# Kernel optimization log

Hardware: AMD Instinct MI355X
Metric: run time of the kernel (lower is better)

## Reference

```python
import jax, jax.numpy as jnp
import numpy as np

B, C, H, W = 4, 128, 64, 64
CQ = C // 2  # channels // reduction_ratio


def setup_inputs() -> dict:
    key = jax.random.key(0)
    ks = jax.random.split(key, 7)
    # kaiming-normal-ish init for 1x1 conv weights (fan_in = C)
    std = float(np.sqrt(2.0 / C))
    return {
        "x": jax.random.normal(ks[0], (B, C, H, W), dtype=jnp.float32),
        "Wq": jax.random.normal(ks[1], (CQ, C), dtype=jnp.float32) * std,
        "bq": jnp.zeros((CQ,), dtype=jnp.float32),
        "Wk": jax.random.normal(ks[2], (CQ, C), dtype=jnp.float32) * std,
        "bk": jnp.zeros((CQ,), dtype=jnp.float32),
        "Wv": jax.random.normal(ks[3], (C, C), dtype=jnp.float32) * std,
        "bv": jnp.zeros((C,), dtype=jnp.float32),
    }


def reference(x, Wq, bq, Wk, bk, Wv, bv):
    b, c, h, w = x.shape
    n = h * w
    xf = x.reshape(b, c, n)  # [B, C, N]
    # 1x1 convs == channel matmuls
    q = jnp.einsum("oc,bcn->bon", Wq, xf) + bq[None, :, None]  # [B, Cq, N]
    k = jnp.einsum("oc,bcn->bon", Wk, xf) + bk[None, :, None]  # [B, Cq, N]
    v = jnp.einsum("oc,bcn->bon", Wv, xf) + bv[None, :, None]  # [B, C, N]
    # scores[b, i, j] = sum_c q[b, c, i] * k[b, c, j]
    scores = jnp.einsum("bci,bcj->bij", q, k)  # [B, N, N]
    probs = jax.nn.softmax(scores, axis=-1)
    # out[b, c, i] = sum_j v[b, c, j] * probs[b, i, j]
    out = jnp.einsum("bcj,bij->bci", v, probs)
    return out.reshape(b, c, h, w)
```

## Files before the change

kernel.cpp:

```cpp
#include <hip/hip_runtime.h>

#define Bn  4
#define Cn  128
#define CQn 64
#define Nn  4096

typedef _Float16 h8_t __attribute__((ext_vector_type(8)));
typedef __fp16   p2_t __attribute__((ext_vector_type(2)));
typedef float    f32x4 __attribute__((ext_vector_type(4)));
typedef unsigned int u32;


#define QKV_BYTES   8388608ull
#define PART_PER_S  4194304ull
#define ML_PER_S    131072ull
#define LOG2E       1.44269504f

__global__ __launch_bounds__(256) void qkv_proj(
    const float* __restrict__ x,
    const float* __restrict__ Wq, const float* __restrict__ bq,
    const float* __restrict__ Wk, const float* __restrict__ bk,
    const float* __restrict__ Wv, const float* __restrict__ bv,
    _Float16* __restrict__ Qh, _Float16* __restrict__ Kh, _Float16* __restrict__ Vg)
{
    __shared__ _Float16 XsT[64][136];

    const int nt   = blockIdx.x;
    const int ot   = blockIdx.y;
    const int b    = blockIdx.z;
    const int tid  = threadIdx.x;
    const int w    = tid >> 6;
    const int lane = tid & 63;
    const int g    = lane >> 4;
    const int ln   = lane & 15;
    const int nbase = nt * 64;

    const float* xb = x + (size_t)b * Cn * Nn + nbase;
    #pragma unroll
    for (int u = 0; u < 8; ++u) {
        int f  = tid + u * 256;
        int c  = f >> 4;
        int n4 = (f & 15) * 4;
        float4 v = *(const float4*)&xb[(size_t)c * Nn + n4];
        XsT[n4 + 0][c] = (_Float16)v.x;
        XsT[n4 + 1][c] = (_Float16)v.y;
        XsT[n4 + 2][c] = (_Float16)v.z;
        XsT[n4 + 3][c] = (_Float16)v.w;
    }
    __syncthreads();

    const float* Wsrc; const float* bsrc;
    if      (ot == 0) { Wsrc = Wq;            bsrc = bq;      }
    else if (ot == 1) { Wsrc = Wk;            bsrc = bk;      }
    else if (ot == 2) { Wsrc = Wv;            bsrc = bv;      }
    else              { Wsrc = Wv + 64 * Cn;  bsrc = bv + 64; }

    union H8 { h8_t h; _Float16 e[8]; };

    const int os = w;
    f32x4 acc[4];
    #pragma unroll
    for (int ns = 0; ns < 4; ++ns) acc[ns] = (f32x4){0.f, 0.f, 0.f, 0.f};

    #pragma unroll
    for (int kc = 0; kc < 4; ++kc) {
        const float* wp = Wsrc + (size_t)(os * 16 + ln) * Cn + kc * 32 + 8 * g;
        float4 wa = *(const float4*)wp;
        float4 wb = *(const float4*)(wp + 4);
        H8 t;
        t.e[0] = (_Float16)wa.x; t.e[1] = (_Float16)wa.y;
        t.e[2] = (_Float16)wa.z; t.e[3] = (_Float16)wa.w;
        t.e[4] = (_Float16)wb.x; t.e[5] = (_Float16)wb.y;
        t.e[6] = (_Float16)wb.z; t.e[7] = (_Float16)wb.w;
        const h8_t wf = t.h;
        #pragma unroll
        for (int ns = 0; ns < 4; ++ns) {
            const h8_t xv = *(const h8_t*)&XsT[ns * 16 + ln][kc * 32 + 8 * g];
            acc[ns] = __builtin_amdgcn_mfma_f32_16x16x32_f16(wf, xv, acc[ns], 0, 0, 0);
        }
    }

    if (ot <= 1) {
        union H4 { _Float16 e[4]; short4 s; };
        _Float16* dst = (ot == 0 ? Qh : Kh) + ((size_t)b * Nn + nbase) * CQn;
        const float sc = (ot == 0) ? LOG2E : 1.f;
        float4 bb = *(const float4*)&bsrc[os * 16 + 4 * g];
        #pragma unroll
        for (int ns = 0; ns < 4; ++ns) {
            H4 h;
            h.e[0] = (_Float16)((acc[ns][0] + bb.x) * sc);
            h.e[1] = (_Float16)((acc[ns][1] + bb.y) * sc);
            h.e[2] = (_Float16)((acc[ns][2] + bb.z) * sc);
            h.e[3] = (_Float16)((acc[ns][3] + bb.w) * sc);
            *(short4*)&dst[(size_t)(ns * 16 + ln) * CQn + os * 16 + 4 * g] = h.s;
        }
    } else {
        _Float16* dst = Vg + (size_t)(b * 64 + nt) * 8192;
        const int cbase = (ot - 2) * 64 + os * 16 + 4 * g;
        #pragma unroll
        for (int ns = 0; ns < 4; ++ns) {
            const int pos = 32 * (ns >> 1) + 8 * ((4 * ns + (ln >> 2)) & 3)
                          + 4 * (ns & 1) + (ln & 3);
            #pragma unroll
            for (int r = 0; r < 4; ++r) {
                dst[(size_t)(cbase + r) * 64 + pos] =
                    (_Float16)(acc[ns][r] + bsrc[os * 16 + 4 * g + r]);
            }
        }
    }
}

__device__ __forceinline__ void gload16(const void* g, void* l) {
    __builtin_amdgcn_global_load_lds(
        (const __attribute__((address_space(1))) u32*)g,
        (__attribute__((address_space(3))) u32*)l, 16, 0, 0);
}

#define KOFF0 0
#define KOFF1 8192
#define VOFF  16384

__global__ __launch_bounds__(256) void attn_split(
    const _Float16* __restrict__ Qh, const _Float16* __restrict__ Kh,
    const _Float16* __restrict__ Vg, float* __restrict__ out,
    _Float16* __restrict__ pPart, float* __restrict__ pMl, int S)
{
    __shared__ __align__(16) char smem[32768];

    const int tid  = threadIdx.x;
    const int w    = tid >> 6;
    const int lane = tid & 63;
    const int g    = lane >> 4;
    const int ln   = lane & 15;
    const int it   = blockIdx.x;
    const int b    = blockIdx.y;
    const int s    = blockIdx.z;
    const int wib  = it * 64 + w * 16;
    const int njt  = 64 / S;

    const _Float16* qrow = Qh + ((size_t)(b * Nn + wib + ln)) * CQn + 8 * g;
    const h8_t q0 = *(const h8_t*)(qrow);
    const h8_t q1 = *(const h8_t*)(qrow + 32);

    const _Float16* Kb  = Kh + (size_t)b * Nn * CQn;
    const _Float16* Vgb = Vg + (size_t)b * 64 * 8192;

    int ks[2];
    #pragma unroll
    for (int u = 0; u < 2; ++u) {
        int G   = u * 256 + tid;
        int row = G >> 3;
        ks[u] = row * CQn + (((G & 7) ^ (row & 7)) * 8);
    }
    int vs[4];
    #pragma unroll
    for (int u = 0; u < 4; ++u) {
        int G   = u * 256 + tid;
        int row = G >> 3;
        vs[u] = row * 64 + (((G & 7) ^ (row & 7)) * 8);
    }

    const int r7  = ln & 7;
    const int kb0 = ln * 128 + (((    g) ^ r7) << 4);
    const int kb1 = ln * 128 + (((4 + g) ^ r7) << 4);

    auto stageK = [&](int koff, int jt) {
        const _Float16* src = Kb + (size_t)jt * 64 * CQn;
        #pragma unroll
        for (int u = 0; u < 2; ++u)
            gload16(src + ks[u], smem + koff + u * 4096 + w * 1024);
    };
    auto stageV = [&](int jt) {
        const _Float16* src = Vgb + (size_t)jt * 8192;
        #pragma unroll
        for (int u = 0; u < 4; ++u)
            gload16(src + vs[u], smem + VOFF + u * 4096 + w * 1024);
    };

    f32x4 oacc[8];
    #pragma unroll
    for (int i = 0; i < 8; ++i) oacc[i] = (f32x4){0.f, 0.f, 0.f, 0.f};
    float m_run = -3.0e38f, l_run = 0.f;

    const int jt0 = s * njt;
    stageK(KOFF0, jt0);
    stageV(jt0);
    __syncthreads();

    for (int t = 0; t < njt; ++t) {
        if (t + 1 < njt) stageK((t & 1) ? KOFF0 : KOFF1, jt0 + t + 1);

        const char* KU = smem + ((t & 1) ? KOFF1 : KOFF0);
        f32x4 st[4];
        __builtin_amdgcn_s_setprio(1);
        #pragma unroll
        for (int js = 0; js < 4; ++js) {
            h8_t k0 = *(const h8_t*)(KU + kb0 + js * 2048);
            h8_t k1 = *(const h8_t*)(KU + kb1 + js * 2048);
            st[js] = (f32x4){0.f, 0.f, 0.f, 0.f};
            st[js] = __builtin_amdgcn_mfma_f32_16x16x32_f16(k0, q0, st[js], 0, 0, 0);
            st[js] = __builtin_amdgcn_mfma_f32_16x16x32_f16(k1, q1, st[js], 0, 0, 0);
        }
        __builtin_amdgcn_s_setprio(0);

        float tmax = st[0][0];
        #pragma unroll
        for (int js = 0; js < 4; ++js)
            #pragma unroll
            for (int r = 0; r < 4; ++r) tmax = fmaxf(tmax, st[js][r]);
        tmax = fmaxf(tmax, __shfl_xor(tmax, 16));
        tmax = fmaxf(tmax, __shfl_xor(tmax, 32));
        if (__any(tmax > m_run + 11.54f)) {
            const float mnew  = fmaxf(m_run, tmax);
            const float alpha = __builtin_amdgcn_exp2f(m_run - mnew);
            const float a0 = __shfl(alpha, 4 * g + 0);
            const float a1 = __shfl(alpha, 4 * g + 1);
            const float a2 = __shfl(alpha, 4 * g + 2);
            const float a3 = __shfl(alpha, 4 * g + 3);
            #pragma unroll
            for (int cs = 0; cs < 8; ++cs) {
                oacc[cs][0] *= a0; oacc[cs][1] *= a1;
                oacc[cs][2] *= a2; oacc[cs][3] *= a3;
            }
            l_run *= alpha;
            m_run = mnew;
        }
        float ts = 0.f;
        #pragma unroll
        for (int js = 0; js < 4; ++js)
            #pragma unroll
            for (int r = 0; r < 4; ++r) {
                float p = __builtin_amdgcn_exp2f(st[js][r] - m_run);
                st[js][r] = p;
                ts += p;
            }
        ts += __shfl_xor(ts, 16);
        ts += __shfl_xor(ts, 32);
        l_run += ts;

        union H8P { h8_t h; p2_t p2[4]; };
        H8P p0u, p1u;
        p0u.p2[0] = __builtin_amdgcn_cvt_pkrtz(st[0][0], st[0][1]);
        p0u.p2[1] = __builtin_amdgcn_cvt_pkrtz(st[0][2], st[0][3]);
        p0u.p2[2] = __builtin_amdgcn_cvt_pkrtz(st[1][0], st[1][1]);
        p0u.p2[3] = __builtin_amdgcn_cvt_pkrtz(st[1][2], st[1][3]);
        p1u.p2[0] = __builtin_amdgcn_cvt_pkrtz(st[2][0], st[2][1]);
        p1u.p2[1] = __builtin_amdgcn_cvt_pkrtz(st[2][2], st[2][3]);
        p1u.p2[2] = __builtin_amdgcn_cvt_pkrtz(st[3][0], st[3][1]);
        p1u.p2[3] = __builtin_amdgcn_cvt_pkrtz(st[3][2], st[3][3]);
        const h8_t pa0 = p0u.h;
        const h8_t pa1 = p1u.h;

        __syncthreads();

        __builtin_amdgcn_s_setprio(1);
        #pragma unroll
        for (int cs = 0; cs < 8; ++cs) {
            h8_t v01 = *(const h8_t*)(smem + VOFF + kb0 + cs * 2048);
            h8_t v23 = *(const h8_t*)(smem + VOFF + kb1 + cs * 2048);
            oacc[cs] = __builtin_amdgcn_mfma_f32_16x16x32_f16(pa0, v01, oacc[cs], 0, 0, 0);
            oacc[cs] = __builtin_amdgcn_mfma_f32_16x16x32_f16(pa1, v23, oacc[cs], 0, 0, 0);
        }
        __builtin_amdgcn_s_setprio(0);

        __syncthreads();

        if (t + 1 < njt) stageV(jt0 + t + 1);
    }

    const float lr = 1.f / l_run;
    const float l0 = __shfl(lr, 4 * g + 0);
    const float l1 = __shfl(lr, 4 * g + 1);
    const float l2 = __shfl(lr, 4 * g + 2);
    const float l3 = __shfl(lr, 4 * g + 3);

    if (S == 1) {
        float* ob = out + (size_t)b * Cn * Nn;
        #pragma unroll
        for (int cs = 0; cs < 8; ++cs) {
            float4 o;
            o.x = oacc[cs][0] * l0;
            o.y = oacc[cs][1] * l1;
            o.z = oacc[cs][2] * l2;
            o.w = oacc[cs][3] * l3;
            *(float4*)&ob[(size_t)(cs * 16 + ln) * Nn + wib + 4 * g] = o;
        }
    } else {
        union H4 { _Float16 e[4]; short4 sv; };
        _Float16* pp = pPart + (((size_t)b * 64 + it) * S + s) * 8192;
        const int qloc = w * 16 + 4 * g;
        #pragma unroll
        for (int cs = 0; cs < 8; ++cs) {
            H4 h;
            h.e[0] = (_Float16)(oacc[cs][0] * l0);
            h.e[1] = (_Float16)(oacc[cs][1] * l1);
            h.e[2] = (_Float16)(oacc[cs][2] * l2);
            h.e[3] = (_Float16)(oacc[cs][3] * l3);
            *(short4*)&pp[(size_t)(cs * 16 + ln) * 64 + qloc] = h.sv;
        }
        if (g == 0) {
            float* ml = pMl + ((((size_t)b * 64 + it) * S + s) * 64 + w * 16 + ln) * 2;
            ml[0] = m_run;
            ml[1] = l_run;
        }
    }
}

__global__ __launch_bounds__(256) void attn_combine(
    const _Float16* __restrict__ pPart, const float* __restrict__ pMl,
    float* __restrict__ out, int S)
{
    const int it  = blockIdx.x;
    const int b   = blockIdx.y;
    const int ch  = blockIdx.z;
    const int tid = threadIdx.x;

    __shared__ float wgt[4][64];
    __shared__ float linv[64];

    if (tid < 64) {
        const float* mlb = pMl + (((size_t)b * 64 + it) * S * 64 + tid) * 2;
        float ms[4], ls[4], m = -3.0e38f;
        for (int s = 0; s < S; ++s) {
            ms[s] = mlb[s * 128 + 0];
            ls[s] = mlb[s * 128 + 1];
            m = fmaxf(m, ms[s]);
        }
        float l = 0.f;
        for (int s = 0; s < S; ++s) {
            float wv = ls[s] * __builtin_amdgcn_exp2f(ms[s] - m);
            wgt[s][tid] = wv;
            l += wv;
        }
        linv[tid] = 1.f / l;
    }
    __syncthreads();

    const int c  = ch * 64 + (tid >> 2);
    const int q0 = (tid & 3) * 16;
    const _Float16* base = pPart + ((size_t)b * 64 + it) * S * 8192 + (size_t)c * 64 + q0;

    float acc[16];
    #pragma unroll
    for (int k = 0; k < 16; ++k) acc[k] = 0.f;
    for (int s = 0; s < S; ++s) {
        const _Float16* ps = base + (size_t)s * 8192;
        #pragma unroll
        for (int k = 0; k < 16; k += 8) {
            h8_t v = *(const h8_t*)(ps + k);
            #pragma unroll
            for (int j = 0; j < 8; ++j)
                acc[k + j] += wgt[s][q0 + k + j] * (float)v[j];
        }
    }
    float* ob = out + ((size_t)b * Cn + c) * Nn + it * 64 + q0;
    #pragma unroll
    for (int k = 0; k < 16; k += 4) {
        float4 o;
        o.x = acc[k + 0] * linv[q0 + k + 0];
        o.y = acc[k + 1] * linv[q0 + k + 1];
        o.z = acc[k + 2] * linv[q0 + k + 2];
        o.w = acc[k + 3] * linv[q0 + k + 3];
        *(float4*)&ob[k] = o;
    }
}

extern "C" void kernel_launch(void* const* d_in, const int* in_sizes, int n_in,
                              void* d_out, int out_size, void* d_ws, size_t ws_size,
                              hipStream_t stream) {
    const float* x  = (const float*)d_in[0];
    const float* Wq = (const float*)d_in[1];
    const float* bq = (const float*)d_in[2];
    const float* Wk = (const float*)d_in[3];
    const float* bk = (const float*)d_in[4];
    const float* Wv = (const float*)d_in[5];
    const float* bv = (const float*)d_in[6];
    float* out = (float*)d_out;

    _Float16* ws = (_Float16*)d_ws;
    _Float16* Qh = ws;
    _Float16* Kh = ws + 1048576;
    _Float16* Vg = ws + 2097152;

    int S = 1;
    if (ws_size >= QKV_BYTES + 4 * (PART_PER_S + ML_PER_S)) S = 4;
    else if (ws_size >= QKV_BYTES + 2 * (PART_PER_S + ML_PER_S)) S = 2;

    _Float16* pPart = (_Float16*)((char*)d_ws + QKV_BYTES);
    float*    pMl   = (float*)((char*)d_ws + QKV_BYTES + (size_t)S * PART_PER_S);

    dim3 gproj(Nn / 64, 4, Bn);
    qkv_proj<<<gproj, 256, 0, stream>>>(x, Wq, bq, Wk, bk, Wv, bv, Qh, Kh, Vg);

    dim3 gattn(Nn / 64, Bn, S);
    attn_split<<<gattn, 256, 0, stream>>>(Qh, Kh, Vg, out, pPart, pMl, S);

    if (S > 1) {
        dim3 gcomb(Nn / 64, Bn, 2);
        attn_combine<<<gcomb, 256, 0, stream>>>(pPart, pMl, out, S);
    }
}
```

Measured before the change: 66.22 us.

## Load V fragments directly from global into registers instead of staging through LDS

Removes the LDS staging of V tiles and instead has each lane read its V fragments straight from global memory, issuing the loads early, before the softmax work, so their latency overlaps it. This drops one of the two barriers per iteration and the LDS write/read traffic for V. In exchange it adds register pressure for 16 h8 vectors, relies on global/L2 latency being hidden, and loses cross-wave sharing of V via LDS, since all four waves read the same V tile. The smem size was also enlarged even though V no longer uses it.

```diff
diff --git a/kernel.cpp b/kernel.cpp
--- a/kernel.cpp
+++ b/kernel.cpp
@@ -118,14 +118,13 @@
 
 #define KOFF0 0
 #define KOFF1 8192
-#define VOFF  16384
 
 __global__ __launch_bounds__(256) void attn_split(
     const _Float16* __restrict__ Qh, const _Float16* __restrict__ Kh,
     const _Float16* __restrict__ Vg, float* __restrict__ out,
     _Float16* __restrict__ pPart, float* __restrict__ pMl, int S)
 {
-    __shared__ __align__(16) char smem[32768];
+    __shared__ __align__(16) char smem[36864];
 
     const int tid  = threadIdx.x;
     const int w    = tid >> 6;
@@ -152,13 +151,6 @@
         int row = G >> 3;
         ks[u] = row * CQn + (((G & 7) ^ (row & 7)) * 8);
     }
-    int vs[4];
-    #pragma unroll
-    for (int u = 0; u < 4; ++u) {
-        int G   = u * 256 + tid;
-        int row = G >> 3;
-        vs[u] = row * 64 + (((G & 7) ^ (row & 7)) * 8);
-    }
 
     const int r7  = ln & 7;
     const int kb0 = ln * 128 + (((    g) ^ r7) << 4);
@@ -170,12 +162,6 @@
         for (int u = 0; u < 2; ++u)
             gload16(src + ks[u], smem + koff + u * 4096 + w * 1024);
     };
-    auto stageV = [&](int jt) {
-        const _Float16* src = Vgb + (size_t)jt * 8192;
-        #pragma unroll
-        for (int u = 0; u < 4; ++u)
-            gload16(src + vs[u], smem + VOFF + u * 4096 + w * 1024);
-    };
 
     f32x4 oacc[8];
     #pragma unroll
@@ -184,11 +170,12 @@
 
     const int jt0 = s * njt;
     stageK(KOFF0, jt0);
-    stageV(jt0);
     __syncthreads();
 
     for (int t = 0; t < njt; ++t) {
         if (t + 1 < njt) stageK((t & 1) ? KOFF0 : KOFF1, jt0 + t + 1);
+
+        const _Float16* vt = Vgb + (size_t)(jt0 + t) * 8192 + (size_t)ln * 64 + 8 * g;
 
         const char* KU = smem + ((t & 1) ? KOFF1 : KOFF0);
         f32x4 st[4];
@@ -202,6 +189,13 @@
             st[js] = __builtin_amdgcn_mfma_f32_16x16x32_f16(k1, q1, st[js], 0, 0, 0);
         }
         __builtin_amdgcn_s_setprio(0);
+
+        h8_t va0[4], va1[4];
+        #pragma unroll
+        for (int cs = 0; cs < 4; ++cs) {
+            va0[cs] = *(const h8_t*)(vt + cs * 1024);
+            va1[cs] = *(const h8_t*)(vt + cs * 1024 + 32);
+        }
 
         float tmax = st[0][0];
         #pragma unroll
@@ -251,21 +245,27 @@
         const h8_t pa0 = p0u.h;
         const h8_t pa1 = p1u.h;
 
+        h8_t vb0[4], vb1[4];
+        #pragma unroll
+        for (int cs = 0; cs < 4; ++cs) {
+            vb0[cs] = *(const h8_t*)(vt + (cs + 4) * 1024);
+            vb1[cs] = *(const h8_t*)(vt + (cs + 4) * 1024 + 32);
+        }
+
+        __builtin_amdgcn_s_setprio(1);
+        #pragma unroll
+        for (int cs = 0; cs < 4; ++cs) {
+            oacc[cs] = __builtin_amdgcn_mfma_f32_16x16x32_f16(pa0, va0[cs], oacc[cs], 0, 0, 0);
+            oacc[cs] = __builtin_amdgcn_mfma_f32_16x16x32_f16(pa1, va1[cs], oacc[cs], 0, 0, 0);
+        }
+        #pragma unroll
+        for (int cs = 0; cs < 4; ++cs) {
+            oacc[cs + 4] = __builtin_amdgcn_mfma_f32_16x16x32_f16(pa0, vb0[cs], oacc[cs + 4], 0, 0, 0);
+            oacc[cs + 4] = __builtin_amdgcn_mfma_f32_16x16x32_f16(pa1, vb1[cs], oacc[cs + 4], 0, 0, 0);
+        }
+        __builtin_amdgcn_s_setprio(0);
+
         __syncthreads();
-
-        __builtin_amdgcn_s_setprio(1);
-        #pragma unroll
-        for (int cs = 0; cs < 8; ++cs) {
-            h8_t v01 = *(const h8_t*)(smem + VOFF + kb0 + cs * 2048);
-            h8_t v23 = *(const h8_t*)(smem + VOFF + kb1 + cs * 2048);
-            oacc[cs] = __builtin_amdgcn_mfma_f32_16x16x32_f16(pa0, v01, oacc[cs], 0, 0, 0);
-            oacc[cs] = __builtin_amdgcn_mfma_f32_16x16x32_f16(pa1, v23, oacc[cs], 0, 0, 0);
-        }
-        __builtin_amdgcn_s_setprio(0);
-
-        __syncthreads();
-
-        if (t + 1 < njt) stageV(jt0 + t + 1);
     }
 
     const float lr = 1.f / l_run;
```

Result: slower. 153.9 us (+132.4%).

## Process two 16-row query tiles per wave to reuse K/V LDS loads

Applied to the files above, without the earlier changes.

Each wave now handles 32 query rows (two 16-row sub-tiles with separate softmax state and accumulators), so every K and V fragment read from LDS feeds twice as many MFMAs. The query tile per block doubles to 128, halving the attention grid, and the combine kernel's indexing and grid are adjusted to match. The K prefetch is moved after a barrier that follows the QK^T step. This doubles accumulator register pressure and halves the number of blocks, which may cost occupancy and parallelism on the large CU count. The shared array grows to 40960 bytes while the code still addresses only the first 32768.

```diff
diff --git a/kernel.cpp b/kernel.cpp
--- a/kernel.cpp
+++ b/kernel.cpp
@@ -116,16 +116,15 @@
         (__attribute__((address_space(3))) u32*)l, 16, 0, 0);
 }
 
-#define KOFF0 0
-#define KOFF1 8192
-#define VOFF  16384
+#define KOFF 0
+#define VOFF 16384
 
 __global__ __launch_bounds__(256) void attn_split(
     const _Float16* __restrict__ Qh, const _Float16* __restrict__ Kh,
     const _Float16* __restrict__ Vg, float* __restrict__ out,
     _Float16* __restrict__ pPart, float* __restrict__ pMl, int S)
 {
-    __shared__ __align__(16) char smem[32768];
+    __shared__ __align__(16) char smem[40960];
 
     const int tid  = threadIdx.x;
     const int w    = tid >> 6;
@@ -135,12 +134,15 @@
     const int it   = blockIdx.x;
     const int b    = blockIdx.y;
     const int s    = blockIdx.z;
-    const int wib  = it * 64 + w * 16;
+    const int wib  = it * 128 + w * 32;
     const int njt  = 64 / S;
 
-    const _Float16* qrow = Qh + ((size_t)(b * Nn + wib + ln)) * CQn + 8 * g;
-    const h8_t q0 = *(const h8_t*)(qrow);
-    const h8_t q1 = *(const h8_t*)(qrow + 32);
+    const _Float16* qra = Qh + ((size_t)(b * Nn + wib + ln)) * CQn + 8 * g;
+    const _Float16* qrb = qra + 16 * CQn;
+    const h8_t qA0 = *(const h8_t*)(qra);
+    const h8_t qA1 = *(const h8_t*)(qra + 32);
+    const h8_t qB0 = *(const h8_t*)(qrb);
+    const h8_t qB1 = *(const h8_t*)(qrb + 32);
 
     const _Float16* Kb  = Kh + (size_t)b * Nn * CQn;
     const _Float16* Vgb = Vg + (size_t)b * 64 * 8192;
@@ -177,32 +179,17 @@
             gload16(src + vs[u], smem + VOFF + u * 4096 + w * 1024);
     };
 
-    f32x4 oacc[8];
-    #pragma unroll
-    for (int i = 0; i < 8; ++i) oacc[i] = (f32x4){0.f, 0.f, 0.f, 0.f};
-    float m_run = -3.0e38f, l_run = 0.f;
-
-    const int jt0 = s * njt;
-    stageK(KOFF0, jt0);
-    stageV(jt0);
-    __syncthreads();
-
-    for (int t = 0; t < njt; ++t) {
-        if (t + 1 < njt) stageK((t & 1) ? KOFF0 : KOFF1, jt0 + t + 1);
-
-        const char* KU = smem + ((t & 1) ? KOFF1 : KOFF0);
-        f32x4 st[4];
-        __builtin_amdgcn_s_setprio(1);
-        #pragma unroll
-        for (int js = 0; js < 4; ++js) {
-            h8_t k0 = *(const h8_t*)(KU + kb0 + js * 2048);
-            h8_t k1 = *(const h8_t*)(KU + kb1 + js * 2048);
-            st[js] = (f32x4){0.f, 0.f, 0.f, 0.f};
-            st[js] = __builtin_amdgcn_mfma_f32_16x16x32_f16(k0, q0, st[js], 0, 0, 0);
-            st[js] = __builtin_amdgcn_mfma_f32_16x16x32_f16(k1, q1, st[js], 0, 0, 0);
-        }
-        __builtin_amdgcn_s_setprio(0);
-
+    f32x4 oaccA[8], oaccB[8];
+    #pragma unroll
+    for (int i = 0; i < 8; ++i) {
+        oaccA[i] = (f32x4){0.f, 0.f, 0.f, 0.f};
+        oaccB[i] = (f32x4){0.f, 0.f, 0.f, 0.f};
+    }
+    float mA = -3.0e38f, lA = 0.f;
+    float mB = -3.0e38f, lB = 0.f;
+
+    auto softmax_pack = [&](f32x4 (&st)[4], float& m_run, float& l_run,
+                            f32x4 (&oacc)[8], h8_t& pa0, h8_t& pa1) {
         float tmax = st[0][0];
         #pragma unroll
         for (int js = 0; js < 4; ++js)
@@ -248,18 +235,49 @@
         p1u.p2[1] = __builtin_amdgcn_cvt_pkrtz(st[2][2], st[2][3]);
         p1u.p2[2] = __builtin_amdgcn_cvt_pkrtz(st[3][0], st[3][1]);
         p1u.p2[3] = __builtin_amdgcn_cvt_pkrtz(st[3][2], st[3][3]);
-        const h8_t pa0 = p0u.h;
-        const h8_t pa1 = p1u.h;
+        pa0 = p0u.h;
+        pa1 = p1u.h;
+    };
+
+    const int jt0 = s * njt;
+    stageK(KOFF, jt0);
+    stageV(jt0);
+    __syncthreads();
+
+    for (int t = 0; t < njt; ++t) {
+        const char* KU = smem + KOFF + ((t & 1) ? 8192 : 0);
+        f32x4 stA[4], stB[4];
+        __builtin_amdgcn_s_setprio(1);
+        #pragma unroll
+        for (int js = 0; js < 4; ++js) {
+            h8_t k0 = *(const h8_t*)(KU + kb0 + js * 2048);
+            h8_t k1 = *(const h8_t*)(KU + kb1 + js * 2048);
+            stA[js] = (f32x4){0.f, 0.f, 0.f, 0.f};
+            stA[js] = __builtin_amdgcn_mfma_f32_16x16x32_f16(k0, qA0, stA[js], 0, 0, 0);
+            stA[js] = __builtin_amdgcn_mfma_f32_16x16x32_f16(k1, qA1, stA[js], 0, 0, 0);
+            stB[js] = (f32x4){0.f, 0.f, 0.f, 0.f};
+            stB[js] = __builtin_amdgcn_mfma_f32_16x16x32_f16(k0, qB0, stB[js], 0, 0, 0);
+            stB[js] = __builtin_amdgcn_mfma_f32_16x16x32_f16(k1, qB1, stB[js], 0, 0, 0);
+        }
+        __builtin_amdgcn_s_setprio(0);
 
         __syncthreads();
+
+        if (t + 1 < njt) stageK(KOFF + ((t & 1) ? 0 : 8192), jt0 + t + 1);
+
+        h8_t paA0, paA1, paB0, paB1;
+        softmax_pack(stA, mA, lA, oaccA, paA0, paA1);
+        softmax_pack(stB, mB, lB, oaccB, paB0, paB1);
 
         __builtin_amdgcn_s_setprio(1);
         #pragma unroll
         for (int cs = 0; cs < 8; ++cs) {
             h8_t v01 = *(const h8_t*)(smem + VOFF + kb0 + cs * 2048);
             h8_t v23 = *(const h8_t*)(smem + VOFF + kb1 + cs * 2048);
-            oacc[cs] = __builtin_amdgcn_mfma_f32_16x16x32_f16(pa0, v01, oacc[cs], 0, 0, 0);
-            oacc[cs] = __builtin_amdgcn_mfma_f32_16x16x32_f16(pa1, v23, oacc[cs], 0, 0, 0);
+            oaccA[cs] = __builtin_amdgcn_mfma_f32_16x16x32_f16(paA0, v01, oaccA[cs], 0, 0, 0);
+            oaccA[cs] = __builtin_amdgcn_mfma_f32_16x16x32_f16(paA1, v23, oaccA[cs], 0, 0, 0);
+            oaccB[cs] = __builtin_amdgcn_mfma_f32_16x16x32_f16(paB0, v01, oaccB[cs], 0, 0, 0);
+            oaccB[cs] = __builtin_amdgcn_mfma_f32_16x16x32_f16(paB1, v23, oaccB[cs], 0, 0, 0);
         }
         __builtin_amdgcn_s_setprio(0);
 
@@ -268,42 +286,46 @@
         if (t + 1 < njt) stageV(jt0 + t + 1);
     }
 
-    const float lr = 1.f / l_run;
-    const float l0 = __shfl(lr, 4 * g + 0);
-    const float l1 = __shfl(lr, 4 * g + 1);
-    const float l2 = __shfl(lr, 4 * g + 2);
-    const float l3 = __shfl(lr, 4 * g + 3);
-
-    if (S == 1) {
-        float* ob = out + (size_t)b * Cn * Nn;
-        #pragma unroll
-        for (int cs = 0; cs < 8; ++cs) {
-            float4 o;
-            o.x = oacc[cs][0] * l0;
-            o.y = oacc[cs][1] * l1;
-            o.z = oacc[cs][2] * l2;
-            o.w = oacc[cs][3] * l3;
-            *(float4*)&ob[(size_t)(cs * 16 + ln) * Nn + wib + 4 * g] = o;
-        }
-    } else {
-        union H4 { _Float16 e[4]; short4 sv; };
-        _Float16* pp = pPart + (((size_t)b * 64 + it) * S + s) * 8192;
-        const int qloc = w * 16 + 4 * g;
-        #pragma unroll
-        for (int cs = 0; cs < 8; ++cs) {
-            H4 h;
-            h.e[0] = (_Float16)(oacc[cs][0] * l0);
-            h.e[1] = (_Float16)(oacc[cs][1] * l1);
-            h.e[2] = (_Float16)(oacc[cs][2] * l2);
-            h.e[3] = (_Float16)(oacc[cs][3] * l3);
-            *(short4*)&pp[(size_t)(cs * 16 + ln) * 64 + qloc] = h.sv;
-        }
-        if (g == 0) {
-            float* ml = pMl + ((((size_t)b * 64 + it) * S + s) * 64 + w * 16 + ln) * 2;
-            ml[0] = m_run;
-            ml[1] = l_run;
-        }
-    }
+    auto epilogue = [&](f32x4 (&oacc)[8], float m_run, float l_run, int h) {
+        const float lr = 1.f / l_run;
+        const float l0 = __shfl(lr, 4 * g + 0);
+        const float l1 = __shfl(lr, 4 * g + 1);
+        const float l2 = __shfl(lr, 4 * g + 2);
+        const float l3 = __shfl(lr, 4 * g + 3);
+        if (S == 1) {
+            float* ob = out + (size_t)b * Cn * Nn;
+            #pragma unroll
+            for (int cs = 0; cs < 8; ++cs) {
+                float4 o;
+                o.x = oacc[cs][0] * l0;
+                o.y = oacc[cs][1] * l1;
+                o.z = oacc[cs][2] * l2;
+                o.w = oacc[cs][3] * l3;
+                *(float4*)&ob[(size_t)(cs * 16 + ln) * Nn + wib + 16 * h + 4 * g] = o;
+            }
+        } else {
+            union H4 { _Float16 e[4]; short4 sv; };
+            _Float16* pp = pPart + (((size_t)b * 32 + it) * S + s) * 16384;
+            const int qloc = w * 32 + 16 * h + 4 * g;
+            #pragma unroll
+            for (int cs = 0; cs < 8; ++cs) {
+                H4 hh;
+                hh.e[0] = (_Float16)(oacc[cs][0] * l0);
+                hh.e[1] = (_Float16)(oacc[cs][1] * l1);
+                hh.e[2] = (_Float16)(oacc[cs][2] * l2);
+                hh.e[3] = (_Float16)(oacc[cs][3] * l3);
+                *(short4*)&pp[(size_t)(cs * 16 + ln) * 128 + qloc] = hh.sv;
+            }
+            if (g == 0) {
+                float* ml = pMl + ((((size_t)b * 32 + it) * S + s) * 128
+                                   + w * 32 + 16 * h + ln) * 2;
+                ml[0] = m_run;
+                ml[1] = l_run;
+            }
+        }
+    };
+    epilogue(oaccA, mA, lA, 0);
+    epilogue(oaccB, mB, lB, 1);
 }
 
 __global__ __launch_bounds__(256) void attn_combine(
@@ -315,15 +337,15 @@
     const int ch  = blockIdx.z;
     const int tid = threadIdx.x;
 
-    __shared__ float wgt[4][64];
-    __shared__ float linv[64];
-
-    if (tid < 64) {
-        const float* mlb = pMl + (((size_t)b * 64 + it) * S * 64 + tid) * 2;
+    __shared__ float wgt[4][128];
+    __shared__ float linv[128];
+
+    if (tid < 128) {
+        const float* mlb = pMl + (((size_t)b * 32 + it) * S * 128 + tid) * 2;
         float ms[4], ls[4], m = -3.0e38f;
         for (int s = 0; s < S; ++s) {
-            ms[s] = mlb[s * 128 + 0];
-            ls[s] = mlb[s * 128 + 1];
+            ms[s] = mlb[s * 256 + 0];
+            ls[s] = mlb[s * 256 + 1];
             m = fmaxf(m, ms[s]);
         }
         float l = 0.f;
@@ -336,15 +358,15 @@
     }
     __syncthreads();
 
-    const int c  = ch * 64 + (tid >> 2);
-    const int q0 = (tid & 3) * 16;
-    const _Float16* base = pPart + ((size_t)b * 64 + it) * S * 8192 + (size_t)c * 64 + q0;
+    const int c  = ch * 32 + (tid >> 3);
+    const int q0 = (tid & 7) * 16;
+    const _Float16* base = pPart + ((size_t)b * 32 + it) * S * 16384 + (size_t)c * 128 + q0;
 
     float acc[16];
     #pragma unroll
     for (int k = 0; k < 16; ++k) acc[k] = 0.f;
     for (int s = 0; s < S; ++s) {
-        const _Float16* ps = base + (size_t)s * 8192;
+        const _Float16* ps = base + (size_t)s * 16384;
         #pragma unroll
         for (int k = 0; k < 16; k += 8) {
             h8_t v = *(const h8_t*)(ps + k);
@@ -353,7 +375,7 @@
                 acc[k + j] += wgt[s][q0 + k + j] * (float)v[j];
         }
     }
-    float* ob = out + ((size_t)b * Cn + c) * Nn + it * 64 + q0;
+    float* ob = out + ((size_t)b * Cn + c) * Nn + it * 128 + q0;
     #pragma unroll
     for (int k = 0; k < 16; k += 4) {
         float4 o;
@@ -392,11 +414,11 @@
     dim3 gproj(Nn / 64, 4, Bn);
     qkv_proj<<<gproj, 256, 0, stream>>>(x, Wq, bq, Wk, bk, Wv, bv, Qh, Kh, Vg);
 
-    dim3 gattn(Nn / 64, Bn, S);
+    dim3 gattn(Nn / 128, Bn, S);
     attn_split<<<gattn, 256, 0, stream>>>(Qh, Kh, Vg, out, pPart, pMl, S);
 
     if (S > 1) {
-        dim3 gcomb(Nn / 64, Bn, 2);
+        dim3 gcomb(Nn / 128, Bn, 4);
         attn_combine<<<gcomb, 256, 0, stream>>>(pPart, pMl, out, S);
     }
 }
```

Measured after the change: 65.87 us. About the same (-0.5%).
